# Kernel tuning notes

Measured on AMD Instinct MI355X. Metric: run time of the kernel, lower is better.

Reference implementation:

```python
import jax, jax.numpy as jnp
import numpy as np

P = 9  # patch_size

def _conv3d(x, w, b):
    # x: (B,C,D,H,W), w: (O,I,3,3,3) -> SAME conv, stride 1
    out = jax.lax.conv_general_dilated(
        x, w, window_strides=(1, 1, 1), padding='SAME',
        dimension_numbers=('NCDHW', 'OIDHW', 'NCDHW'))
    return out + b[None, :, None, None, None]

def _unfold(z):
    # z: (C, D, HW) with D % P == 0 and HW % P == 0.
    # nn.Unfold(kernel=(P,P), stride=(P,P)) on a (1,1,D,HW) image is an exact
    # non-overlapping tiling -> pure reshape. Returns (C, L, P*P) with the
    # patch flattened row-major (kh, kw), matching torch's unfold layout.
    C, D, HW = z.shape
    z = z.reshape(C, D // P, P, HW // P, P)
    return z.transpose(0, 1, 3, 2, 4).reshape(C, (D // P) * (HW // P), P * P)

def _res_trans(t, W1, W2):
    # Linear(81->162, no bias) -> Linear(162->81, no bias) -> LeakyReLU(0.2)
    return jax.nn.leaky_relu(jnp.einsum('clk,ok->clo', jnp.einsum('clp,hp->clh', t, W1), W2), 0.2)

def setup_inputs() -> dict:
    key = jax.random.key(0)
    ks = jax.random.split(key, 8)
    B, C, D, H, W = 1, 32, 36, 48, 48
    s = 0.05
    return {
        'x':  jax.random.normal(ks[0], (B, C, D, H, W), jnp.float32),
        'y':  jax.random.normal(ks[1], (B, C, D, H, W), jnp.float32),
        'Wx': jax.random.normal(ks[2], (C, C, 3, 3, 3), jnp.float32) * s,
        'bx': jax.random.normal(ks[3], (C,), jnp.float32) * s,
        'Wy': jax.random.normal(ks[4], (C, C, 3, 3, 3), jnp.float32) * s,
        'by': jax.random.normal(ks[5], (C,), jnp.float32) * s,
        'W1': jax.random.normal(ks[6], (2 * P * P, P * P), jnp.float32) * s,
        'W2': jax.random.normal(ks[7], (P * P, 2 * P * P), jnp.float32) * s,
    }

def reference(x, y, Wx, bx, Wy, by, W1, W2):
    xc = _conv3d(x, Wx, bx)  # (1,C,D,H,W)
    yc = _conv3d(y, Wy, by)
    _, C, D, H, Wd = xc.shape
    xr = xc.reshape(C, D, H * Wd)
    yr = yc.reshape(C, D, H * Wd)
    a = _res_trans(_unfold(xr), W1, W2)  # (C, L, 81)
    b = _res_trans(_unfold(yr), W1, W2)  # (C, L, 81)
    # torch: matmul(unfold_img(L,81), trans(unfold_feamap).T(81,L)) / 81
    att = jnp.einsum('clp,cmp->clm', a, b) / (P * P)  # (C, L, L)
    return att[None]  # (1, C, L, L)
```

## Files before the change

kernel.cpp:

```cpp
#include <hip/hip_runtime.h>
#include <hip/hip_bf16.h>

typedef __attribute__((ext_vector_type(8))) short short8;
typedef __attribute__((ext_vector_type(4))) float f32x4;


static __device__ __forceinline__ unsigned short f2bf(float f) {
    unsigned int u = __float_as_uint(f);
    unsigned int r = (u + 0x7fffu + ((u >> 16) & 1u)) >> 16;
    return (unsigned short)r;
}

__global__ __launch_bounds__(256) void setup_kernel(
    const float* __restrict__ x, const float* __restrict__ y,
    const float* __restrict__ W1, const float* __restrict__ W2,
    const float* __restrict__ Wx, const float* __restrict__ Wy,
    unsigned short* __restrict__ xt, unsigned short* __restrict__ Mo,
    unsigned short* __restrict__ Wbf, unsigned short* __restrict__ tbuf) {
    int bb = blockIdx.x, tid = threadIdx.x;
    if (bb < 3800) {
        int img = bb / 1900, rr = bb % 1900;
        int dd = rr / 50, hh = rr % 50;
        unsigned short* dst = xt + img*(38*50*50*32) + (dd*50 + hh)*(50*32);
        if (dd >= 1 && dd <= 36 && hh >= 1 && hh <= 48) {
            __shared__ unsigned short lds[48*33];
            int d = dd - 1, h = hh - 1;
            const float* src = img ? y : x;
            #pragma unroll
            for (int i = 0; i < 6; ++i) {
                int idx = tid + 256*i;
                int ci = idx / 48, w = idx % 48;
                lds[w*33 + ci] = f2bf(src[((ci*36 + d)*48 + h)*48 + w]);
            }
            __syncthreads();
            #pragma unroll
            for (int i = 0; i < 7; ++i) {
                int idx = tid + 256*i;
                if (idx < 1600) {
                    int wp = idx >> 5, ci = idx & 31;
                    unsigned short v = (wp == 0 || wp == 49) ? (unsigned short)0
                                                             : lds[(wp-1)*33 + ci];
                    dst[idx] = v;
                }
            }
        } else {
            #pragma unroll
            for (int i = 0; i < 7; ++i) {
                int idx = tid + 256*i;
                if (idx < 1600) dst[idx] = 0;
            }
        }
    } else if (bb < 3836) {
        int gid = (bb - 3800)*256 + tid;
        int o = gid / 96, p = gid % 96;
        float v = 0.f;
        if (o < 81 && p < 81) {
            for (int k = 0; k < 162; ++k) v += W2[o*162 + k] * W1[k*81 + p];
        }
        Mo[o*96 + p] = f2bf(v);
    } else if (bb < 4052) {
        int e = (bb - 3836)*256 + tid;
        if (e < 2*27*32*32) {
            int ci  = e % 32;
            int co  = (e / 32) % 32;
            int tap = (e / 1024) % 27;
            int img = e / 27648;
            const float* src = img ? Wy : Wx;
            Wbf[e] = f2bf(src[co*864 + ci*27 + tap]);
        }
    } else {
        int row = (bb - 4052)*256 + tid;
        unsigned short* tr = tbuf + row*96 + 81;
        #pragma unroll
        for (int j = 0; j < 15; ++j) tr[j] = 0;
    }
}

__global__ __launch_bounds__(256) void conv_kernel(
    const unsigned short* __restrict__ xt,
    const float* __restrict__ bx, const float* __restrict__ by,
    const unsigned short* __restrict__ Wbf, unsigned short* __restrict__ tbuf) {
    int b = blockIdx.x;
    int img = b / 216; int rr = b % 216;
    int d0 = rr / 6; int hb = rr % 6;
    int tid = threadIdx.x, wv = tid >> 6, lane = tid & 63;
    int r16 = lane & 15, g4 = lane >> 4;
    int hbase = hb*8 + wv*2;
    const unsigned short* Ximg = xt + img*(38*50*50*32);
    const unsigned short* Wimg = Wbf + img*(27*32*32);
    const float* bias = img ? by : bx;

    f32x4 acc[2][3][2];
    #pragma unroll
    for (int i = 0; i < 2; ++i)
        #pragma unroll
        for (int j = 0; j < 3; ++j)
            #pragma unroll
            for (int k = 0; k < 2; ++k) acc[i][j][k] = (f32x4){0.f, 0.f, 0.f, 0.f};

    #pragma unroll 1
    for (int kd = 0; kd < 3; ++kd) {
        short8 wf[3][3][2];
        #pragma unroll
        for (int kh = 0; kh < 3; ++kh)
            #pragma unroll
            for (int kw = 0; kw < 3; ++kw)
                #pragma unroll
                for (int ct = 0; ct < 2; ++ct)
                    wf[kh][kw][ct] = *reinterpret_cast<const short8*>(
                        Wimg + (((kd*3 + kh)*3 + kw)*32 + ct*16 + r16)*32 + 8*g4);
        #pragma unroll
        for (int r = 0; r < 4; ++r) {
            const unsigned short* xrow = Ximg + ((d0 + kd)*50 + (hbase + r))*(50*32);
            #pragma unroll
            for (int kw = 0; kw < 3; ++kw) {
                short8 bfr[3];
                #pragma unroll
                for (int wt = 0; wt < 3; ++wt)
                    bfr[wt] = *reinterpret_cast<const short8*>(xrow + (wt*16 + r16 + kw)*32 + 8*g4);
                #pragma unroll
                for (int hh = 0; hh < 2; ++hh) {
                    int kh = r - hh;
                    if (kh >= 0 && kh < 3) {
                        #pragma unroll
                        for (int wt = 0; wt < 3; ++wt) {
                            acc[0][wt][hh] = __builtin_amdgcn_mfma_f32_16x16x32_bf16(wf[kh][kw][0], bfr[wt], acc[0][wt][hh], 0, 0, 0);
                            acc[1][wt][hh] = __builtin_amdgcn_mfma_f32_16x16x32_bf16(wf[kh][kw][1], bfr[wt], acc[1][wt][hh], 0, 0, 0);
                        }
                    }
                }
            }
        }
    }

    int l_hi = (d0/9)*256, p_hi = (d0%9)*9;
    unsigned short* tb = tbuf + img*(32*1024*96);
    #pragma unroll
    for (int hh = 0; hh < 2; ++hh) {
        int h = hbase + hh;
        #pragma unroll
        for (int ct = 0; ct < 2; ++ct)
            #pragma unroll
            for (int wt = 0; wt < 3; ++wt)
                #pragma unroll
                for (int r = 0; r < 4; ++r) {
                    int co = ct*16 + g4*4 + r;
                    int w  = wt*16 + r16;
                    float v = acc[ct][wt][hh][r] + bias[co];
                    int hw = h*48 + w;
                    int l = l_hi + hw/9, p = p_hi + hw%9;
                    tb[(co*1024 + l)*96 + p] = f2bf(v);
                }
    }
}

__global__ __launch_bounds__(256) void rt_kernel(const unsigned short* __restrict__ tbuf,
                                                 const unsigned short* __restrict__ Mo,
                                                 unsigned short* __restrict__ ab) {
    int b = blockIdx.x;
    int img = b >> 7, c = (b >> 2) & 31, mc = b & 3;
    int tid = threadIdx.x, wv = tid >> 6, lane = tid & 63;
    int r16 = lane & 15, g4 = lane >> 4;

    short8 Bf[3][6];
    #pragma unroll
    for (int ks = 0; ks < 3; ++ks)
        #pragma unroll
        for (int n = 0; n < 6; ++n)
            Bf[ks][n] = *reinterpret_cast<const short8*>(Mo + (n*16 + r16)*96 + ks*32 + 8*g4);

    const unsigned short* tc = tbuf + (img*32 + c)*(1024*96);
    unsigned short*       oc = ab   + (img*32 + c)*(1024*96);
    for (int q = 0; q < 4; ++q) {
        int rowb = (mc*16 + wv*4 + q) * 16;
        f32x4 acc[6];
        #pragma unroll
        for (int n = 0; n < 6; ++n) acc[n] = (f32x4){0.f, 0.f, 0.f, 0.f};
        #pragma unroll
        for (int ks = 0; ks < 3; ++ks) {
            short8 Af = *reinterpret_cast<const short8*>(tc + (rowb + r16)*96 + ks*32 + 8*g4);
            #pragma unroll
            for (int n = 0; n < 6; ++n)
                acc[n] = __builtin_amdgcn_mfma_f32_16x16x32_bf16(Af, Bf[ks][n], acc[n], 0, 0, 0);
        }
        #pragma unroll
        for (int n = 0; n < 6; ++n)
            #pragma unroll
            for (int r = 0; r < 4; ++r) {
                int row = rowb + g4*4 + r;
                float v = acc[n][r];
                v = v > 0.f ? v : 0.2f*v;
                oc[row*96 + n*16 + r16] = f2bf(v);
            }
    }
}

__global__ __launch_bounds__(256) void att_kernel(const unsigned short* __restrict__ ab,
                                                  float* __restrict__ out) {
    int bid = blockIdx.x;
    int b = (bid & 7) * 256 + (bid >> 3);
    int c = b >> 6, ty = (b >> 3) & 7, tx = b & 7;
    int tid = threadIdx.x, wv = tid >> 6, lane = tid & 63;
    int r16 = lane & 15, g4 = lane >> 4;
    const unsigned short* arow = ab + c*(1024*96);
    const unsigned short* brow = ab + (32 + c)*(1024*96);
    int rb = ty*128 + wv*32;
    int cb = tx*128;
    f32x4 acc[2][8];
    #pragma unroll
    for (int m = 0; m < 2; ++m)
        #pragma unroll
        for (int n = 0; n < 8; ++n) acc[m][n] = (f32x4){0.f, 0.f, 0.f, 0.f};

    #pragma unroll
    for (int ks = 0; ks < 3; ++ks) {
        short8 A0 = *reinterpret_cast<const short8*>(arow + (rb +      r16)*96 + ks*32 + 8*g4);
        short8 A1 = *reinterpret_cast<const short8*>(arow + (rb + 16 + r16)*96 + ks*32 + 8*g4);
        #pragma unroll
        for (int n = 0; n < 8; ++n) {
            short8 Bf = *reinterpret_cast<const short8*>(brow + (cb + n*16 + r16)*96 + ks*32 + 8*g4);
            acc[0][n] = __builtin_amdgcn_mfma_f32_16x16x32_bf16(A0, Bf, acc[0][n], 0, 0, 0);
            acc[1][n] = __builtin_amdgcn_mfma_f32_16x16x32_bf16(A1, Bf, acc[1][n], 0, 0, 0);
        }
    }
    const float s = 1.f / 81.f;
    #pragma unroll
    for (int mt = 0; mt < 2; ++mt)
        #pragma unroll
        for (int n = 0; n < 8; ++n)
            #pragma unroll
            for (int r = 0; r < 4; ++r) {
                int row = rb + mt*16 + g4*4 + r;
                int col = cb + n*16 + r16;
                out[(c*1024 + row)*1024 + col] = acc[mt][n][r] * s;
            }
}

extern "C" void kernel_launch(void* const* d_in, const int* in_sizes, int n_in,
                              void* d_out, int out_size, void* d_ws, size_t ws_size,
                              hipStream_t stream) {
    const float* x  = (const float*)d_in[0];
    const float* y  = (const float*)d_in[1];
    const float* Wx = (const float*)d_in[2];
    const float* bx = (const float*)d_in[3];
    const float* Wy = (const float*)d_in[4];
    const float* by = (const float*)d_in[5];
    const float* W1 = (const float*)d_in[6];
    const float* W2 = (const float*)d_in[7];
    (void)in_sizes; (void)n_in; (void)out_size; (void)ws_size;

    char* ws = (char*)d_ws;
    unsigned short* xt   = (unsigned short*)(ws);
    unsigned short* abuf = (unsigned short*)(ws);
    unsigned short* tbuf = (unsigned short*)(ws + 12582912);
    unsigned short* Mo   = (unsigned short*)(ws + 25165824);
    unsigned short* Wbf  = (unsigned short*)(ws + 25184256);
    float* out = (float*)d_out;

    setup_kernel<<<4308, 256, 0, stream>>>(x, y, W1, W2, Wx, Wy, xt, Mo, Wbf, tbuf);
    conv_kernel<<<432, 256, 0, stream>>>(xt, bx, by, Wbf, tbuf);
    rt_kernel<<<256, 256, 0, stream>>>(tbuf, Mo, abuf);
    att_kernel<<<2048, 256, 0, stream>>>(abuf, out);
}
```

Baseline: 86.79 us.

## Split conv output channels across waves and spread rt_kernel over more blocks

The conv kernel now runs 512-thread blocks in which each wave computes only one 16-channel half of the output channels. This halves the accumulator and weight registers per wave and doubles the number of waves in flight. Block indices are also remapped, interleaving by eight, so neighbouring blocks land on different XCDs. The rt kernel drops its four-iteration inner loop and launches four times as many blocks, each handling 64 rows. The cost is that the input row fragments are now loaded redundantly by two waves, and each rt block reloads its B fragments for less work.

```diff
diff --git a/kernel.cpp b/kernel.cpp
--- a/kernel.cpp
+++ b/kernel.cpp
@@ -76,39 +76,37 @@
     }
 }
 
-__global__ __launch_bounds__(256) void conv_kernel(
+__global__ __launch_bounds__(512) void conv_kernel(
     const unsigned short* __restrict__ xt,
     const float* __restrict__ bx, const float* __restrict__ by,
     const unsigned short* __restrict__ Wbf, unsigned short* __restrict__ tbuf) {
     int b = blockIdx.x;
-    int img = b / 216; int rr = b % 216;
+    int wg = (b & 7) * 54 + (b >> 3);
+    int img = wg / 216; int rr = wg % 216;
     int d0 = rr / 6; int hb = rr % 6;
     int tid = threadIdx.x, wv = tid >> 6, lane = tid & 63;
+    int hp = wv >> 1, ct = wv & 1;
     int r16 = lane & 15, g4 = lane >> 4;
-    int hbase = hb*8 + wv*2;
+    int hbase = hb*8 + hp*2;
     const unsigned short* Ximg = xt + img*(38*50*50*32);
     const unsigned short* Wimg = Wbf + img*(27*32*32);
     const float* bias = img ? by : bx;
 
-    f32x4 acc[2][3][2];
-    #pragma unroll
-    for (int i = 0; i < 2; ++i)
-        #pragma unroll
-        for (int j = 0; j < 3; ++j)
-            #pragma unroll
-            for (int k = 0; k < 2; ++k) acc[i][j][k] = (f32x4){0.f, 0.f, 0.f, 0.f};
+    f32x4 acc[3][2];
+    #pragma unroll
+    for (int j = 0; j < 3; ++j)
+        #pragma unroll
+        for (int k = 0; k < 2; ++k) acc[j][k] = (f32x4){0.f, 0.f, 0.f, 0.f};
 
     #pragma unroll 1
     for (int kd = 0; kd < 3; ++kd) {
-        short8 wf[3][3][2];
+        short8 wf[3][3];
         #pragma unroll
         for (int kh = 0; kh < 3; ++kh)
             #pragma unroll
             for (int kw = 0; kw < 3; ++kw)
-                #pragma unroll
-                for (int ct = 0; ct < 2; ++ct)
-                    wf[kh][kw][ct] = *reinterpret_cast<const short8*>(
-                        Wimg + (((kd*3 + kh)*3 + kw)*32 + ct*16 + r16)*32 + 8*g4);
+                wf[kh][kw] = *reinterpret_cast<const short8*>(
+                    Wimg + (((kd*3 + kh)*3 + kw)*32 + ct*16 + r16)*32 + 8*g4);
         #pragma unroll
         for (int r = 0; r < 4; ++r) {
             const unsigned short* xrow = Ximg + ((d0 + kd)*50 + (hbase + r))*(50*32);
@@ -123,10 +121,8 @@
                     int kh = r - hh;
                     if (kh >= 0 && kh < 3) {
                         #pragma unroll
-                        for (int wt = 0; wt < 3; ++wt) {
-                            acc[0][wt][hh] = __builtin_amdgcn_mfma_f32_16x16x32_bf16(wf[kh][kw][0], bfr[wt], acc[0][wt][hh], 0, 0, 0);
-                            acc[1][wt][hh] = __builtin_amdgcn_mfma_f32_16x16x32_bf16(wf[kh][kw][1], bfr[wt], acc[1][wt][hh], 0, 0, 0);
-                        }
+                        for (int wt = 0; wt < 3; ++wt)
+                            acc[wt][hh] = __builtin_amdgcn_mfma_f32_16x16x32_bf16(wf[kh][kw], bfr[wt], acc[wt][hh], 0, 0, 0);
                     }
                 }
             }
@@ -139,18 +135,16 @@
     for (int hh = 0; hh < 2; ++hh) {
         int h = hbase + hh;
         #pragma unroll
-        for (int ct = 0; ct < 2; ++ct)
-            #pragma unroll
-            for (int wt = 0; wt < 3; ++wt)
-                #pragma unroll
-                for (int r = 0; r < 4; ++r) {
-                    int co = ct*16 + g4*4 + r;
-                    int w  = wt*16 + r16;
-                    float v = acc[ct][wt][hh][r] + bias[co];
-                    int hw = h*48 + w;
-                    int l = l_hi + hw/9, p = p_hi + hw%9;
-                    tb[(co*1024 + l)*96 + p] = f2bf(v);
-                }
+        for (int wt = 0; wt < 3; ++wt)
+            #pragma unroll
+            for (int r = 0; r < 4; ++r) {
+                int co = ct*16 + g4*4 + r;
+                int w  = wt*16 + r16;
+                float v = acc[wt][hh][r] + bias[co];
+                int hw = h*48 + w;
+                int l = l_hi + hw/9, p = p_hi + hw%9;
+                tb[(co*1024 + l)*96 + p] = f2bf(v);
+            }
     }
 }
 
@@ -158,7 +152,7 @@
                                                  const unsigned short* __restrict__ Mo,
                                                  unsigned short* __restrict__ ab) {
     int b = blockIdx.x;
-    int img = b >> 7, c = (b >> 2) & 31, mc = b & 3;
+    int img = b >> 9, c = (b >> 4) & 31, seg = b & 15;
     int tid = threadIdx.x, wv = tid >> 6, lane = tid & 63;
     int r16 = lane & 15, g4 = lane >> 4;
 
@@ -171,28 +165,26 @@
 
     const unsigned short* tc = tbuf + (img*32 + c)*(1024*96);
     unsigned short*       oc = ab   + (img*32 + c)*(1024*96);
-    for (int q = 0; q < 4; ++q) {
-        int rowb = (mc*16 + wv*4 + q) * 16;
-        f32x4 acc[6];
-        #pragma unroll
-        for (int n = 0; n < 6; ++n) acc[n] = (f32x4){0.f, 0.f, 0.f, 0.f};
-        #pragma unroll
-        for (int ks = 0; ks < 3; ++ks) {
-            short8 Af = *reinterpret_cast<const short8*>(tc + (rowb + r16)*96 + ks*32 + 8*g4);
-            #pragma unroll
-            for (int n = 0; n < 6; ++n)
-                acc[n] = __builtin_amdgcn_mfma_f32_16x16x32_bf16(Af, Bf[ks][n], acc[n], 0, 0, 0);
-        }
+    int rowb = seg*64 + wv*16;
+    f32x4 acc[6];
+    #pragma unroll
+    for (int n = 0; n < 6; ++n) acc[n] = (f32x4){0.f, 0.f, 0.f, 0.f};
+    #pragma unroll
+    for (int ks = 0; ks < 3; ++ks) {
+        short8 Af = *reinterpret_cast<const short8*>(tc + (rowb + r16)*96 + ks*32 + 8*g4);
         #pragma unroll
         for (int n = 0; n < 6; ++n)
-            #pragma unroll
-            for (int r = 0; r < 4; ++r) {
-                int row = rowb + g4*4 + r;
-                float v = acc[n][r];
-                v = v > 0.f ? v : 0.2f*v;
-                oc[row*96 + n*16 + r16] = f2bf(v);
-            }
-    }
+            acc[n] = __builtin_amdgcn_mfma_f32_16x16x32_bf16(Af, Bf[ks][n], acc[n], 0, 0, 0);
+    }
+    #pragma unroll
+    for (int n = 0; n < 6; ++n)
+        #pragma unroll
+        for (int r = 0; r < 4; ++r) {
+            int row = rowb + g4*4 + r;
+            float v = acc[n][r];
+            v = v > 0.f ? v : 0.2f*v;
+            oc[row*96 + n*16 + r16] = f2bf(v);
+        }
 }
 
 __global__ __launch_bounds__(256) void att_kernel(const unsigned short* __restrict__ ab,
@@ -258,7 +250,7 @@
     float* out = (float*)d_out;
 
     setup_kernel<<<4308, 256, 0, stream>>>(x, y, W1, W2, Wx, Wy, xt, Mo, Wbf, tbuf);
-    conv_kernel<<<432, 256, 0, stream>>>(xt, bx, by, Wbf, tbuf);
-    rt_kernel<<<256, 256, 0, stream>>>(tbuf, Mo, abuf);
+    conv_kernel<<<432, 512, 0, stream>>>(xt, bx, by, Wbf, tbuf);
+    rt_kernel<<<1024, 256, 0, stream>>>(tbuf, Mo, abuf);
     att_kernel<<<2048, 256, 0, stream>>>(abuf, out);
 }
```

Result: slower. 96.87 us (+11.6%).
